# Performance work log

Hardware: AMD Instinct MI355X
Metric: run time of the kernel (lower is better)

## Reference

```python
import jax, jax.numpy as jnp
import numpy as np

B, S, HID, H = 2, 2048, 1024, 16
D = HID // H
ROTARY_BASE = 10000.0
LN_EPS = 1e-5
NEG = -1e9


def setup_inputs() -> dict:
    key = jax.random.key(0)
    ks = jax.random.split(key, 20)
    w = lambda k, shape: (jax.random.normal(k, shape, jnp.float32) * 0.02)
    return {
        "x": jax.random.normal(ks[0], (B, S, HID), jnp.float32),
        "mask": jnp.ones((B, S), jnp.int32),
        "wq": w(ks[1], (HID, HID)), "bq": jnp.zeros((HID,), jnp.float32),
        "wk": w(ks[2], (HID, HID)), "bk": jnp.zeros((HID,), jnp.float32),
        "wv": w(ks[3], (HID, HID)), "bv": jnp.zeros((HID,), jnp.float32),
        "wo": w(ks[4], (HID, HID)), "bo": jnp.zeros((HID,), jnp.float32),
        "w1": w(ks[5], (HID, 4 * HID)), "b1": jnp.zeros((4 * HID,), jnp.float32),
        "w2": w(ks[6], (4 * HID, HID)), "b2": jnp.zeros((HID,), jnp.float32),
        "ln1_g": jnp.ones((HID,), jnp.float32), "ln1_b": jnp.zeros((HID,), jnp.float32),
        "ln2_g": jnp.ones((HID,), jnp.float32), "ln2_b": jnp.zeros((HID,), jnp.float32),
    }


def _layer_norm(z, g, b):
    m = z.mean(-1, keepdims=True)
    v = ((z - m) ** 2).mean(-1, keepdims=True)
    return (z - m) / jnp.sqrt(v + LN_EPS) * g + b


def _rope(t, cos, sin):
    # t: [B,H,S,D]; even/odd halves rotated then CONCATENATED (matches source, not interleaved)
    e, o = t[..., 0::2], t[..., 1::2]
    return jnp.concatenate([e * cos - o * sin, e * sin + o * cos], axis=-1)


def reference(x, mask, wq, bq, wk, bk, wv, bv, wo, bo, w1, b1, w2, b2,
              ln1_g, ln1_b, ln2_g, ln2_b):
    b, s, hid = x.shape
    h, d = H, D
    # rotary tables for positions [0, s)
    inv_freq = 1.0 / (ROTARY_BASE ** (jnp.arange(0, d, 2, dtype=jnp.float32) / d))
    freqs = jnp.arange(s, dtype=jnp.float32)[:, None] * inv_freq[None, :]  # [S, D/2]
    cos = jnp.cos(freqs)[None, None]  # [1,1,S,D/2]
    sin = jnp.sin(freqs)[None, None]

    # ---- attention sublayer (pre-norm) ----
    xn = _layer_norm(x, ln1_g, ln1_b)
    q = (xn @ wq + bq).reshape(b, s, h, d).transpose(0, 2, 1, 3)
    k = (xn @ wk + bk).reshape(b, s, h, d).transpose(0, 2, 1, 3)
    v = (xn @ wv + bv).reshape(b, s, h, d).transpose(0, 2, 1, 3)
    q = _rope(q, cos, sin)
    k = _rope(k, cos, sin)

    scores = jnp.einsum('bhqd,bhkd->bhqk', q, k) / np.sqrt(d).astype(np.float32)
    pad = (mask == 0)[:, None, None, :]              # [B,1,1,S]
    scores = jnp.where(pad, NEG, scores)
    causal = jnp.triu(jnp.ones((s, s), bool), 1)     # [S,S]
    scores = jnp.where(causal, NEG, scores)
    probs = jax.nn.softmax(scores, axis=-1)          # dropout p=0.0 (eval)
    ctx = jnp.einsum('bhqk,bhkd->bhqd', probs, v)
    ctx = ctx.transpose(0, 2, 1, 3).reshape(b, s, hid)
    attn_out = ctx @ wo + bo
    x = x + attn_out

    # ---- FFN sublayer (pre-norm) ----
    xn = _layer_norm(x, ln2_g, ln2_b)
    f = jax.nn.gelu(xn @ w1 + b1, approximate=True) @ w2 + b2
    return x + f
```

## Files before the change

kernel.cpp:

```cpp
#include <hip/hip_runtime.h>

typedef unsigned short u16;
typedef unsigned int u32;
typedef __attribute__((ext_vector_type(8))) u16 u16x8;
typedef __attribute__((ext_vector_type(4))) u16 u16x4;
typedef __attribute__((ext_vector_type(8))) __bf16 bf16x8;
typedef __attribute__((ext_vector_type(4))) float f32x4;

static __device__ __forceinline__ float bf2f(u16 u) {
    union { u32 i; float f; } v; v.i = ((u32)u) << 16; return v.f;
}
static __device__ __forceinline__ u16 f2bf(float f) {
    union { float f; u32 i; } v; v.f = f;
    u32 r = v.i + 0x7fffu + ((v.i >> 16) & 1u);
    return (u16)(r >> 16);
}
static __device__ __forceinline__ u16 f2bfn(float f) {
    __bf16 h = (__bf16)f;
    return *(u16*)&h;
}
static __device__ __forceinline__ void gl_lds16(const void* gsrc, void* ldst) {
    __builtin_amdgcn_global_load_lds((const __attribute__((address_space(1))) void*)gsrc,
                                     (__attribute__((address_space(3))) void*)ldst, 16, 0, 0);
}

__global__ __launch_bounds__(256) void transpose_cvt(const float* __restrict__ in,
                                                     u16* __restrict__ out, int K, int N) {
    __shared__ float t[32][33];
    int k0 = blockIdx.y << 5, n0 = blockIdx.x << 5;
    int r = threadIdx.x >> 3, c4 = threadIdx.x & 7;
    float4 v = *(const float4*)(in + (size_t)(k0 + r) * N + n0 + (c4 << 2));
    t[r][c4 * 4 + 0] = v.x; t[r][c4 * 4 + 1] = v.y;
    t[r][c4 * 4 + 2] = v.z; t[r][c4 * 4 + 3] = v.w;
    __syncthreads();
    u16x4 o;
    o[0] = f2bf(t[c4 * 4 + 0][r]); o[1] = f2bf(t[c4 * 4 + 1][r]);
    o[2] = f2bf(t[c4 * 4 + 2][r]); o[3] = f2bf(t[c4 * 4 + 3][r]);
    *(u16x4*)(out + (size_t)(n0 + r) * K + k0 + (c4 << 2)) = o;
}

__global__ __launch_bounds__(256) void transpose_cvt4(const float* __restrict__ w0, const float* __restrict__ w1,
                                                      const float* __restrict__ w2, const float* __restrict__ w3,
                                                      u16* __restrict__ o0, u16* __restrict__ o1,
                                                      u16* __restrict__ o2, u16* __restrict__ o3) {
    __shared__ float t[32][33];
    const float* in; u16* out;
    switch (blockIdx.z) {
        case 0:  in = w0; out = o0; break;
        case 1:  in = w1; out = o1; break;
        case 2:  in = w2; out = o2; break;
        default: in = w3; out = o3; break;
    }
    int k0 = blockIdx.y << 5, n0 = blockIdx.x << 5;
    int r = threadIdx.x >> 3, c4 = threadIdx.x & 7;
    float4 v = *(const float4*)(in + (size_t)(k0 + r) * 1024 + n0 + (c4 << 2));
    t[r][c4 * 4 + 0] = v.x; t[r][c4 * 4 + 1] = v.y;
    t[r][c4 * 4 + 2] = v.z; t[r][c4 * 4 + 3] = v.w;
    __syncthreads();
    u16x4 o;
    o[0] = f2bf(t[c4 * 4 + 0][r]); o[1] = f2bf(t[c4 * 4 + 1][r]);
    o[2] = f2bf(t[c4 * 4 + 2][r]); o[3] = f2bf(t[c4 * 4 + 3][r]);
    *(u16x4*)(out + (size_t)(n0 + r) * 1024 + k0 + (c4 << 2)) = o;
}

__global__ void concat_bias(const float* __restrict__ bq, const float* __restrict__ bk,
                            const float* __restrict__ bv, float* __restrict__ bqkv,
                            const int* __restrict__ mask, float* __restrict__ maskf) {
    int i = blockIdx.x * 256 + threadIdx.x;
    if (i < 3072) {
        float v = (i < 1024) ? bq[i] : (i < 2048 ? bk[i - 1024] : bv[i - 2048]);
        bqkv[i] = v;
    }
    if (i < 4096) maskf[i] = (float)mask[i];
}

__global__ void rope_tab(float* __restrict__ cost, float* __restrict__ sint) {
    int idx = blockIdx.x * 256 + threadIdx.x;
    int s = idx >> 5, f = idx & 31;
    float inv = powf(10000.0f, -((float)(2 * f)) / 64.0f);
    float a = (float)s * inv;
    cost[idx] = cosf(a);
    sint[idx] = sinf(a);
}

__global__ __launch_bounds__(256) void ln_kernel(const float* __restrict__ x,
                                                 const float* __restrict__ gam,
                                                 const float* __restrict__ bet,
                                                 u16* __restrict__ out) {
    int row = blockIdx.x, tid = threadIdx.x;
    float4 v = *((const float4*)(x + (size_t)row * 1024) + tid);
    float s = v.x + v.y + v.z + v.w;
    float sq = v.x * v.x + v.y * v.y + v.z * v.z + v.w * v.w;
    #pragma unroll
    for (int off = 32; off >= 1; off >>= 1) {
        s += __shfl_xor(s, off);
        sq += __shfl_xor(sq, off);
    }
    __shared__ float red[8];
    int wid = tid >> 6, lane = tid & 63;
    if (lane == 0) { red[wid] = s; red[wid + 4] = sq; }
    __syncthreads();
    float ts = red[0] + red[1] + red[2] + red[3];
    float tq = red[4] + red[5] + red[6] + red[7];
    float mean = ts * (1.0f / 1024.0f);
    float var = tq * (1.0f / 1024.0f) - mean * mean;
    float rstd = rsqrtf(var + 1e-5f);
    float4 g = ((const float4*)gam)[tid];
    float4 b = ((const float4*)bet)[tid];
    u16x4 o;
    o[0] = f2bfn((v.x - mean) * rstd * g.x + b.x);
    o[1] = f2bfn((v.y - mean) * rstd * g.y + b.y);
    o[2] = f2bfn((v.z - mean) * rstd * g.z + b.z);
    o[3] = f2bfn((v.w - mean) * rstd * g.w + b.w);
    *(u16x4*)(out + (size_t)row * 1024 + (tid << 2)) = o;
}

__global__ __launch_bounds__(256) void ln_fuse(float* __restrict__ x2, const u16* __restrict__ part,
                                               const float* __restrict__ gam, const float* __restrict__ bet,
                                               u16* __restrict__ out) {
    int row = blockIdx.x, tid = threadIdx.x;
    float4 v = *((const float4*)(x2 + (size_t)row * 1024) + tid);
    u16x4 pv = *(const u16x4*)(part + (size_t)row * 1024 + (tid << 2));
    v.x += bf2f(pv[0]); v.y += bf2f(pv[1]); v.z += bf2f(pv[2]); v.w += bf2f(pv[3]);
    *((float4*)(x2 + (size_t)row * 1024) + tid) = v;
    float s = v.x + v.y + v.z + v.w;
    float sq = v.x * v.x + v.y * v.y + v.z * v.z + v.w * v.w;
    #pragma unroll
    for (int off = 32; off >= 1; off >>= 1) {
        s += __shfl_xor(s, off);
        sq += __shfl_xor(sq, off);
    }
    __shared__ float red[8];
    int wid = tid >> 6, lane = tid & 63;
    if (lane == 0) { red[wid] = s; red[wid + 4] = sq; }
    __syncthreads();
    float ts = red[0] + red[1] + red[2] + red[3];
    float tq = red[4] + red[5] + red[6] + red[7];
    float mean = ts * (1.0f / 1024.0f);
    float var = tq * (1.0f / 1024.0f) - mean * mean;
    float rstd = rsqrtf(var + 1e-5f);
    float4 g = ((const float4*)gam)[tid];
    float4 b = ((const float4*)bet)[tid];
    u16x4 o;
    o[0] = f2bfn((v.x - mean) * rstd * g.x + b.x);
    o[1] = f2bfn((v.y - mean) * rstd * g.y + b.y);
    o[2] = f2bfn((v.z - mean) * rstd * g.z + b.z);
    o[3] = f2bfn((v.w - mean) * rstd * g.w + b.w);
    *(u16x4*)(out + (size_t)row * 1024 + (tid << 2)) = o;
}

template <int EPI>
__global__ __launch_bounds__(512, 2) void gemm256(const u16* __restrict__ A, const u16* __restrict__ Bt,
                                                  const float* __restrict__ bias,
                                                  u16* __restrict__ outb, int M, int N, int K) {
    __shared__ __align__(16) u16 lds[65536];
    const int tid = threadIdx.x;
    const int lane = tid & 63, wid = tid >> 6;
    const int cl = lane & 15, g4 = lane >> 4;
    const int wr = wid >> 2, wc = wid & 3;
    const int gx = gridDim.x;
    const int lid = blockIdx.y * gx + blockIdx.x;
    const int per8 = (gx * gridDim.y) >> 3;
    const int newlin = (lid & 7) * per8 + (lid >> 3);
    const int m0 = (newlin / gx) << 8;
    const int n0 = (newlin % gx) << 8;
    const int NT = K >> 6;
    f32x4 acc[8][4] = {};
    const int r0 = tid >> 3;          const int gc0 = (tid & 7) ^ (r0 & 7);
    const int r1 = (tid + 512) >> 3;  const int gc1 = (tid & 7) ^ (r1 & 7);
    const int wub = wid << 10;

    auto stageHalf = [&](int buf, int mat, int h, int kt) {
        const u16* src = mat ? Bt : A;
        const int base0 = mat ? n0 : m0;
        char* d = (char*)lds + buf * 65536 + mat * 32768 + h * 16384 + wub;
        gl_lds16(src + (size_t)(base0 + h * 128 + r0) * K + (kt << 6) + (gc0 << 3), d);
        gl_lds16(src + (size_t)(base0 + h * 128 + r1) * K + (kt << 6) + (gc1 << 3), d + 8192);
    };

    stageHalf(0, 0, 0, 0); stageHalf(0, 0, 1, 0);
    stageHalf(0, 1, 0, 0); stageHalf(0, 1, 1, 0);
    asm volatile("s_waitcnt vmcnt(0)" ::: "memory");
    __builtin_amdgcn_s_barrier();

    for (int t = 0; t < NT; ++t) {
        const int buf = t & 1, nbuf = buf ^ 1;
        const bool more = (t + 1 < NT);
        const int abase = buf * 65536 + wr * 16384;
        const int bbase = buf * 65536 + 32768 + (wc >> 1) * 16384;
        bf16x8 bfr[4][2];
        #pragma unroll
        for (int q = 0; q < 4; ++q) {
            bf16x8 afr[2][2];
            #pragma unroll
            for (int di = 0; di < 2; ++di)
                #pragma unroll
                for (int ks = 0; ks < 2; ++ks) {
                    int row = q * 32 + di * 16 + cl;
                    int gr = ks * 4 + g4;
                    afr[di][ks] = *(const bf16x8*)((char*)lds + abase + (((row << 3) + (gr ^ (row & 7))) << 4));
                }
            if (q == 0) {
                #pragma unroll
                for (int j = 0; j < 4; ++j)
                    #pragma unroll
                    for (int ks = 0; ks < 2; ++ks) {
                        int row = ((wc & 1) << 6) + j * 16 + cl;
                        int gr = ks * 4 + g4;
                        bfr[j][ks] = *(const bf16x8*)((char*)lds + bbase + (((row << 3) + (gr ^ (row & 7))) << 4));
                    }
            }
            if (more) stageHalf(nbuf, q >> 1, q & 1, t + 1);
            __builtin_amdgcn_s_barrier();
            asm volatile("s_waitcnt lgkmcnt(0)" ::: "memory");
            __builtin_amdgcn_sched_barrier(0);
            __builtin_amdgcn_s_setprio(1);
            #pragma unroll
            for (int di = 0; di < 2; ++di)
                #pragma unroll
                for (int j = 0; j < 4; ++j)
                    #pragma unroll
                    for (int ks = 0; ks < 2; ++ks)
                        acc[q * 2 + di][j] = __builtin_amdgcn_mfma_f32_16x16x32_bf16(
                            afr[di][ks], bfr[j][ks], acc[q * 2 + di][j], 0, 0, 0);
            __builtin_amdgcn_s_setprio(0);
            if (q == 3 && more) asm volatile("s_waitcnt vmcnt(0)" ::: "memory");
            __builtin_amdgcn_s_barrier();
            if (q == 3) __builtin_amdgcn_sched_barrier(0);
        }
    }
    #pragma unroll
    for (int i = 0; i < 8; ++i)
        #pragma unroll
        for (int j = 0; j < 4; ++j) {
            int row = m0 + wr * 128 + i * 16 + g4 * 4;
            int col = n0 + wc * 64 + j * 16 + cl;
            float bc = bias[col];
            #pragma unroll
            for (int rr = 0; rr < 4; ++rr) {
                float v = acc[i][j][rr] + bc;
                size_t idx = (size_t)(row + rr) * N + col;
                if constexpr (EPI == 0) {
                    outb[idx] = f2bfn(v);
                } else {
                    float tg = 0.7978845608f * (v + 0.044715f * v * v * v);
                    outb[idx] = f2bfn(v / (1.0f + exp2f(tg * -2.88539008f)));
                }
            }
        }
}

__global__ __launch_bounds__(512, 2) void gemm256r(const u16* __restrict__ A, const u16* __restrict__ Bt,
                                                   const float* __restrict__ bias,
                                                   const float* __restrict__ res,
                                                   float* __restrict__ outf, u16* __restrict__ poutb,
                                                   int M, int N, int K) {
    __shared__ __align__(16) u16 lds[65536];
    const int tid = threadIdx.x;
    const int lane = tid & 63, wid = tid >> 6;
    const int cl = lane & 15, g4 = lane >> 4;
    const int wr = wid >> 2, wc = wid & 3;
    const int gx = gridDim.x;
    const int lid = blockIdx.y * gx + blockIdx.x;
    const int per8 = (gx * gridDim.y) >> 3;
    const int newlin = (lid & 7) * per8 + (lid >> 3);
    const int m0 = (newlin / gx) << 8;
    const int n0 = (newlin % gx) << 8;
    const int kchunk = K / gridDim.z;
    const int kbase = blockIdx.z * kchunk;
    const int NT = kchunk >> 6;
    f32x4 acc[8][4] = {};
    const int r0 = tid >> 3;          const int gc0 = (tid & 7) ^ (r0 & 7);
    const int r1 = (tid + 512) >> 3;  const int gc1 = (tid & 7) ^ (r1 & 7);
    const int wub = wid << 10;

    auto stageHalf = [&](int buf, int mat, int h, int kt) {
        const u16* src = mat ? Bt : A;
        const int base0 = mat ? n0 : m0;
        char* d = (char*)lds + buf * 65536 + mat * 32768 + h * 16384 + wub;
        gl_lds16(src + (size_t)(base0 + h * 128 + r0) * K + kbase + (kt << 6) + (gc0 << 3), d);
        gl_lds16(src + (size_t)(base0 + h * 128 + r1) * K + kbase + (kt << 6) + (gc1 << 3), d + 8192);
    };

    stageHalf(0, 0, 0, 0); stageHalf(0, 0, 1, 0);
    stageHalf(0, 1, 0, 0); stageHalf(0, 1, 1, 0);
    asm volatile("s_waitcnt vmcnt(0)" ::: "memory");
    __builtin_amdgcn_s_barrier();

    for (int t = 0; t < NT; ++t) {
        const int buf = t & 1, nbuf = buf ^ 1;
        const bool more = (t + 1 < NT);
        const int abase = buf * 65536 + wr * 16384;
        const int bbase = buf * 65536 + 32768 + (wc >> 1) * 16384;
        bf16x8 bfr[4][2];
        #pragma unroll
        for (int q = 0; q < 4; ++q) {
            bf16x8 afr[2][2];
            #pragma unroll
            for (int di = 0; di < 2; ++di)
                #pragma unroll
                for (int ks = 0; ks < 2; ++ks) {
                    int row = q * 32 + di * 16 + cl;
                    int gr = ks * 4 + g4;
                    afr[di][ks] = *(const bf16x8*)((char*)lds + abase + (((row << 3) + (gr ^ (row & 7))) << 4));
                }
            if (q == 0) {
                #pragma unroll
                for (int j = 0; j < 4; ++j)
                    #pragma unroll
                    for (int ks = 0; ks < 2; ++ks) {
                        int row = ((wc & 1) << 6) + j * 16 + cl;
                        int gr = ks * 4 + g4;
                        bfr[j][ks] = *(const bf16x8*)((char*)lds + bbase + (((row << 3) + (gr ^ (row & 7))) << 4));
                    }
            }
            if (more) stageHalf(nbuf, q >> 1, q & 1, t + 1);
            __builtin_amdgcn_s_barrier();
            asm volatile("s_waitcnt lgkmcnt(0)" ::: "memory");
            __builtin_amdgcn_sched_barrier(0);
            __builtin_amdgcn_s_setprio(1);
            #pragma unroll
            for (int di = 0; di < 2; ++di)
                #pragma unroll
                for (int j = 0; j < 4; ++j)
                    #pragma unroll
                    for (int ks = 0; ks < 2; ++ks)
                        acc[q * 2 + di][j] = __builtin_amdgcn_mfma_f32_16x16x32_bf16(
                            afr[di][ks], bfr[j][ks], acc[q * 2 + di][j], 0, 0, 0);
            __builtin_amdgcn_s_setprio(0);
            if (q == 3 && more) asm volatile("s_waitcnt vmcnt(0)" ::: "memory");
            __builtin_amdgcn_s_barrier();
            if (q == 3) __builtin_amdgcn_sched_barrier(0);
        }
    }
    if (blockIdx.z == 0) {
        #pragma unroll
        for (int i = 0; i < 8; ++i)
            #pragma unroll
            for (int j = 0; j < 4; ++j) {
                int row = m0 + wr * 128 + i * 16 + g4 * 4;
                int col = n0 + wc * 64 + j * 16 + cl;
                float bc = bias[col];
                #pragma unroll
                for (int rr = 0; rr < 4; ++rr) {
                    size_t idx = (size_t)(row + rr) * N + col;
                    outf[idx] = acc[i][j][rr] + bc + res[idx];
                }
            }
    } else {
        const size_t pbase = (size_t)(blockIdx.z - 1) * ((size_t)M * N);
        #pragma unroll
        for (int i = 0; i < 8; ++i)
            #pragma unroll
            for (int j = 0; j < 4; ++j) {
                int row = m0 + wr * 128 + i * 16 + g4 * 4;
                int col = n0 + wc * 64 + j * 16 + cl;
                #pragma unroll
                for (int rr = 0; rr < 4; ++rr)
                    poutb[pbase + (size_t)(row + rr) * N + col] = f2bfn(acc[i][j][rr]);
            }
    }
}

template <int EPI>
__global__ __launch_bounds__(256) void gemm_bt(const u16* __restrict__ A, const u16* __restrict__ Bt,
                                               const float* __restrict__ bias,
                                               const float* __restrict__ res,
                                               u16* __restrict__ outb, float* __restrict__ outf,
                                               u16* __restrict__ poutb,
                                               int M, int N, int K) {
    __shared__ __align__(16) u16 As[3][4096];
    __shared__ __align__(16) u16 Bs[3][4096];
    const int tid = threadIdx.x;
    const int lane = tid & 63, wid = tid >> 6;
    const int g = lane >> 4, cl = lane & 15;
    const int wr = wid >> 1, wc = wid & 1;
    const int gx = gridDim.x;
    const int lid = blockIdx.y * gx + blockIdx.x;
    const int per8 = (gx * gridDim.y) >> 3;
    const int newlin = (lid & 7) * per8 + (lid >> 3);
    const int m0 = (newlin / gx) << 7;
    const int n0 = (newlin % gx) << 7;
    const int kchunk = K / gridDim.z;
    const int kbase = blockIdx.z * kchunk;
    const int NT = kchunk >> 5;
    f32x4 acc[4][4] = {};
    const int grow = tid >> 2;
    const int gcol = (tid & 3) ^ ((tid >> 3) & 3);

    auto stage = [&](int buf, int kt) {
        const int ko = kbase + (kt << 5);
        gl_lds16(A + (size_t)(m0 + grow) * K + ko + (gcol << 3),       &As[buf][wid << 9]);
        gl_lds16(A + (size_t)(m0 + grow + 64) * K + ko + (gcol << 3),  &As[buf][(wid << 9) + 2048]);
        gl_lds16(Bt + (size_t)(n0 + grow) * K + ko + (gcol << 3),      &Bs[buf][wid << 9]);
        gl_lds16(Bt + (size_t)(n0 + grow + 64) * K + ko + (gcol << 3), &Bs[buf][(wid << 9) + 2048]);
    };

    stage(0, 0);
    stage(1, 1);
    for (int kt = 0; kt < NT; ++kt) {
        if (kt + 1 < NT) asm volatile("s_waitcnt vmcnt(4)" ::: "memory");
        else             asm volatile("s_waitcnt vmcnt(0)" ::: "memory");
        __builtin_amdgcn_s_barrier();
        __builtin_amdgcn_sched_barrier(0);
        if (kt + 2 < NT) stage((kt + 2) % 3, kt + 2);
        const int cb = kt % 3;
        bf16x8 a[4], b[4];
        #pragma unroll
        for (int i = 0; i < 4; ++i) {
            int row = (wr << 6) + (i << 4) + cl;
            a[i] = *(const bf16x8*)&As[cb][((row << 2) + (g ^ ((row >> 1) & 3))) << 3];
        }
        #pragma unroll
        for (int j = 0; j < 4; ++j) {
            int row = (wc << 6) + (j << 4) + cl;
            b[j] = *(const bf16x8*)&Bs[cb][((row << 2) + (g ^ ((row >> 1) & 3))) << 3];
        }
        __builtin_amdgcn_s_setprio(1);
        #pragma unroll
        for (int i = 0; i < 4; ++i)
            #pragma unroll
            for (int j = 0; j < 4; ++j)
                acc[i][j] = __builtin_amdgcn_mfma_f32_16x16x32_bf16(a[i], b[j], acc[i][j], 0, 0, 0);
        __builtin_amdgcn_s_setprio(0);
    }
    if (blockIdx.z == 0) {
        #pragma unroll
        for (int i = 0; i < 4; ++i)
            #pragma unroll
            for (int j = 0; j < 4; ++j) {
                int row = m0 + (wr << 6) + (i << 4) + (g << 2);
                int col = n0 + (wc << 6) + (j << 4) + cl;
                float bc = bias[col];
                #pragma unroll
                for (int rr = 0; rr < 4; ++rr) {
                    float v = acc[i][j][rr] + bc;
                    size_t idx = (size_t)(row + rr) * N + col;
                    outf[idx] = v + res[idx];
                }
            }
    } else {
        const size_t pbase = (size_t)(blockIdx.z - 1) * ((size_t)M * N);
        #pragma unroll
        for (int i = 0; i < 4; ++i)
            #pragma unroll
            for (int j = 0; j < 4; ++j) {
                int row = m0 + (wr << 6) + (i << 4) + (g << 2);
                int col = n0 + (wc << 6) + (j << 4) + cl;
                #pragma unroll
                for (int rr = 0; rr < 4; ++rr)
                    poutb[pbase + (size_t)(row + rr) * N + col] = f2bfn(acc[i][j][rr]);
            }
    }
}

__global__ __launch_bounds__(256) void reduce_addb(float* __restrict__ out, const u16* __restrict__ p,
                                                   int nparts) {
    int i = blockIdx.x * 256 + threadIdx.x;
    float4 a = ((const float4*)out)[i];
    for (int j = 0; j < nparts; ++j) {
        u16x4 v = *(const u16x4*)(p + (size_t)j * 4194304 + ((size_t)i << 2));
        a.x += bf2f(v[0]); a.y += bf2f(v[1]); a.z += bf2f(v[2]); a.w += bf2f(v[3]);
    }
    ((float4*)out)[i] = a;
}

__global__ __launch_bounds__(256) void rope_qk(const u16* __restrict__ qkv,
                                               const float* __restrict__ cost,
                                               const float* __restrict__ sint,
                                               u16* __restrict__ qr, u16* __restrict__ kr) {
    int tid = threadIdx.x;
    int rowid = (blockIdx.x << 4) + (tid >> 4);
    int j = tid & 15;
    int half = j >> 3, jj = j & 7;
    int b = rowid >> 15;
    int h = (rowid >> 11) & 15;
    int s = rowid & 2047;
    size_t qbase = (size_t)((b << 11) + s) * 3072 + (h << 6);
    float cf[4], sf_[4];
    {
        float4 c = *(const float4*)(cost + (s << 5) + (jj << 2));
        float4 sn = *(const float4*)(sint + (s << 5) + (jj << 2));
        cf[0] = c.x; cf[1] = c.y; cf[2] = c.z; cf[3] = c.w;
        sf_[0] = sn.x; sf_[1] = sn.y; sf_[2] = sn.z; sf_[3] = sn.w;
    }
    size_t obase = (size_t)rowid * 64 + (half << 5) + (jj << 2);
    {
        u16x8 v = *(const u16x8*)(qkv + qbase + (jj << 3));
        u16x4 o;
        #pragma unroll
        for (int m2 = 0; m2 < 4; ++m2) {
            float e = bf2f(v[2 * m2]), od = bf2f(v[2 * m2 + 1]);
            float val = (half == 0) ? (e * cf[m2] - od * sf_[m2]) : (e * sf_[m2] + od * cf[m2]);
            o[m2] = f2bfn(val * 0.1803368801f);
        }
        *(u16x4*)(qr + obase) = o;
    }
    {
        u16x8 v = *(const u16x8*)(qkv + qbase + 1024 + (jj << 3));
        u16x4 o;
        #pragma unroll
        for (int m2 = 0; m2 < 4; ++m2) {
            float e = bf2f(v[2 * m2]), od = bf2f(v[2 * m2 + 1]);
            float val = (half == 0) ? (e * cf[m2] - od * sf_[m2]) : (e * sf_[m2] + od * cf[m2]);
            o[m2] = f2bfn(val);
        }
        *(u16x4*)(kr + obase) = o;
    }
}

__global__ __launch_bounds__(256) void v_transpose(const u16* __restrict__ qkv,
                                                   u16* __restrict__ vt) {
    __shared__ __align__(16) u16 tl[64 * 80];
    int stile = blockIdx.x, bh = blockIdx.y;
    int b = bh >> 4, h = bh & 15;
    int tid = threadIdx.x;
    #pragma unroll
    for (int i = 0; i < 2; ++i) {
        int slot = tid + (i << 8);
        int srow = slot >> 3, c = slot & 7;
        u16x8 v = *(const u16x8*)(qkv + (size_t)((b << 11) + (stile << 6) + srow) * 3072 + 2048 + (h << 6) + (c << 3));
        *(u16x8*)(tl + srow * 80 + (c << 3)) = v;
    }
    __syncthreads();
    #pragma unroll
    for (int i = 0; i < 2; ++i) {
        int slot = tid + (i << 8);
        int drow = slot >> 3, c = slot & 7;
        u16x8 o;
        #pragma unroll
        for (int m2 = 0; m2 < 8; ++m2) o[m2] = tl[(c * 8 + m2) * 80 + drow];
        *(u16x8*)(vt + ((size_t)bh * 64 + drow) * 2048 + (stile << 6) + (c << 3)) = o;
    }
}

__global__ __launch_bounds__(256) void attn_kernel(const u16* __restrict__ Q, const u16* __restrict__ Kd,
                                                   const u16* __restrict__ Vt, const float* __restrict__ maskf,
                                                   u16* __restrict__ ctx) {
    __shared__ __align__(16) u16 Ks[2][4096];
    __shared__ __align__(16) u16 Vs[2][4096];
    __shared__ __align__(16) u16 Ps[4096];
    const int tid = threadIdx.x, lane = tid & 63, w = tid >> 6;
    const int g = lane >> 4, cl = lane & 15;
    const int lid = blockIdx.y * 16 + blockIdx.x;
    const int xcd = lid & 7, slot = lid >> 3;
    const int bh = xcd * 4 + (slot >> 4);
    const int pair = slot & 15;
    const int b = bh >> 4, h = bh & 15;
    const u16* Kb = Kd + (size_t)bh * 2048 * 64;
    const u16* Vb = Vt + (size_t)bh * 64 * 2048;
    const int sr = tid >> 3;
    const int sg = (tid & 7) ^ (sr & 7);
    bf16x8 onesb;
    #pragma unroll
    for (int i2 = 0; i2 < 8; ++i2) onesb[i2] = (__bf16)1.0f;
    char* const pwb = (char*)Ps + w * 2048 + cl * 128 + ((g & 1) << 3);

    #pragma unroll
    for (int ci = 0; ci < 2; ++ci) {
        const int qb = (ci == 0) ? (31 - pair) : pair;
        const size_t qoff = ((size_t)bh * 2048 + qb * 64 + w * 16 + cl) * 64;
        const bf16x8 qa0 = *(const bf16x8*)(Q + qoff + (g << 3));
        const bf16x8 qa1 = *(const bf16x8*)(Q + qoff + 32 + (g << 3));
        const int qrow = qb * 64 + w * 16 + cl;
        f32x4 acc[4] = {};
        f32x4 lsum = {};

        auto stage = [&](int buf, int t) {
            char* kd = (char*)&Ks[buf][0] + (w << 10);
            char* vd = (char*)&Vs[buf][0] + (w << 10);
            const u16* Kg = Kb + (size_t)(t * 64) * 64;
            gl_lds16(Kg + (size_t)sr * 64 + (sg << 3), kd);
            gl_lds16(Kg + (size_t)(sr + 32) * 64 + (sg << 3), kd + 4096);
            gl_lds16(Vb + (size_t)sr * 2048 + t * 64 + (sg << 3), vd);
            gl_lds16(Vb + (size_t)(sr + 32) * 2048 + t * 64 + (sg << 3), vd + 4096);
        };

        __syncthreads();
        stage(0, 0);
        asm volatile("s_waitcnt vmcnt(0)" ::: "memory");
        __syncthreads();

        int cur = 0;
        for (int t = 0; t <= qb; ++t) {
            const bool more = (t < qb);
            if (more) stage(cur ^ 1, t + 1);
            f32x4 sf[4];
            __builtin_amdgcn_s_setprio(1);
            #pragma unroll
            for (int ct = 0; ct < 4; ++ct) {
                f32x4 s = {};
                int krow = ct * 16 + cl;
                bf16x8 kb0 = *(const bf16x8*)((char*)&Ks[cur][0] + krow * 128 + ((g ^ (krow & 7)) << 4));
                bf16x8 kb1 = *(const bf16x8*)((char*)&Ks[cur][0] + krow * 128 + (((4 + g) ^ (krow & 7)) << 4));
                s = __builtin_amdgcn_mfma_f32_16x16x32_bf16(kb0, qa0, s, 0, 0, 0);
                s = __builtin_amdgcn_mfma_f32_16x16x32_bf16(kb1, qa1, s, 0, 0, 0);
                sf[ct] = s;
            }
            __builtin_amdgcn_s_setprio(0);
            const bool diag = (t == qb);
            #pragma unroll
            for (int ct = 0; ct < 4; ++ct) {
                const int kc0 = t * 64 + ct * 16 + (g << 2);
                const float4 mv = *(const float4*)(maskf + (b << 11) + kc0);
                float p0 = exp2f(sf[ct][0]) * mv.x;
                float p1 = exp2f(sf[ct][1]) * mv.y;
                float p2 = exp2f(sf[ct][2]) * mv.z;
                float p3 = exp2f(sf[ct][3]) * mv.w;
                if (diag) {
                    p0 = (kc0 + 0 <= qrow) ? p0 : 0.0f;
                    p1 = (kc0 + 1 <= qrow) ? p1 : 0.0f;
                    p2 = (kc0 + 2 <= qrow) ? p2 : 0.0f;
                    p3 = (kc0 + 3 <= qrow) ? p3 : 0.0f;
                }
                u32 lo, hi;
                asm("v_cvt_pk_bf16_f32 %0, %1, %2" : "=v"(lo) : "v"(p0), "v"(p1));
                asm("v_cvt_pk_bf16_f32 %0, %1, %2" : "=v"(hi) : "v"(p2), "v"(p3));
                uint2 pk; pk.x = lo; pk.y = hi;
                *(uint2*)(pwb + ((((ct << 1) + (g >> 1)) ^ (cl & 7)) << 4)) = pk;
            }
            __builtin_amdgcn_s_setprio(1);
            #pragma unroll
            for (int kc = 0; kc < 2; ++kc) {
                bf16x8 pa = *(const bf16x8*)((char*)Ps + w * 2048 + cl * 128 + (((kc * 4 + g) ^ (cl & 7)) << 4));
                lsum = __builtin_amdgcn_mfma_f32_16x16x32_bf16(pa, onesb, lsum, 0, 0, 0);
                #pragma unroll
                for (int n = 0; n < 4; ++n) {
                    int vrow = n * 16 + cl;
                    bf16x8 vb = *(const bf16x8*)((char*)&Vs[cur][0] + vrow * 128 + (((kc * 4 + g) ^ (vrow & 7)) << 4));
                    acc[n] = __builtin_amdgcn_mfma_f32_16x16x32_bf16(pa, vb, acc[n], 0, 0, 0);
                }
            }
            __builtin_amdgcn_s_setprio(0);
            if (more) {
                asm volatile("s_waitcnt vmcnt(0)" ::: "memory");
                __syncthreads();
            }
            cur ^= 1;
        }
        #pragma unroll
        for (int n = 0; n < 4; ++n)
            #pragma unroll
            for (int rr = 0; rr < 4; ++rr) {
                int token = (b << 11) + qb * 64 + w * 16 + g * 4 + rr;
                int col = (h << 6) + n * 16 + cl;
                ctx[(size_t)token * 1024 + col] = f2bfn(acc[n][rr] / lsum[rr]);
            }
    }
}

extern "C" void kernel_launch(void* const* d_in, const int* in_sizes, int n_in,
                              void* d_out, int out_size, void* d_ws, size_t ws_size,
                              hipStream_t stream) {
    const float* x   = (const float*)d_in[0];
    const int* mask  = (const int*)d_in[1];
    const float* wq  = (const float*)d_in[2];
    const float* bq  = (const float*)d_in[3];
    const float* wk  = (const float*)d_in[4];
    const float* bk  = (const float*)d_in[5];
    const float* wv  = (const float*)d_in[6];
    const float* bv  = (const float*)d_in[7];
    const float* wo  = (const float*)d_in[8];
    const float* bo  = (const float*)d_in[9];
    const float* w1  = (const float*)d_in[10];
    const float* b1  = (const float*)d_in[11];
    const float* w2  = (const float*)d_in[12];
    const float* b2  = (const float*)d_in[13];
    const float* g1  = (const float*)d_in[14];
    const float* be1 = (const float*)d_in[15];
    const float* g2  = (const float*)d_in[16];
    const float* be2 = (const float*)d_in[17];
    float* out = (float*)d_out;
    char* ws = (char*)d_ws;

    u16* wqkvT  = (u16*)(ws + 0);
    u16* woT    = (u16*)(ws + 6291456);
    u16* w1T    = (u16*)(ws + 8388608);
    u16* w2T    = (u16*)(ws + 16777216);
    float* bqkv = (float*)(ws + 25165824);
    float* cost = (float*)(ws + 25178112);
    float* sint = (float*)(ws + 25440256);
    u16* xn     = (u16*)(ws + 25702400);
    float* x2   = (float*)(ws + 34091008);
    float* maskf= (float*)(ws + 34091008);
    u16* qkv    = (u16*)(ws + 50868224);
    u16* ffh    = (u16*)(ws + 50868224);
    u16* qr     = (u16*)(ws + 76034048);
    u16* kr     = (u16*)(ws + 84422656);
    u16* vt     = (u16*)(ws + 92811264);
    u16* ctx    = (u16*)(ws + 101199872);
    u16* partb  = (u16*)(ws + 84422656);

    transpose_cvt4<<<dim3(32, 32, 4), 256, 0, stream>>>(wq, wk, wv, wo,
                                                        wqkvT, wqkvT + 1024 * 1024, wqkvT + 2048 * 1024, woT);
    transpose_cvt<<<dim3(128, 32), 256, 0, stream>>>(w1, w1T, 1024, 4096);
    transpose_cvt<<<dim3(32, 128), 256, 0, stream>>>(w2, w2T, 4096, 1024);
    concat_bias<<<16, 256, 0, stream>>>(bq, bk, bv, bqkv, mask, maskf);
    rope_tab<<<256, 256, 0, stream>>>(cost, sint);

    ln_kernel<<<4096, 256, 0, stream>>>(x, g1, be1, xn);
    gemm256<0><<<dim3(12, 16), 512, 0, stream>>>(xn, wqkvT, bqkv, qkv, 4096, 3072, 1024);
    rope_qk<<<4096, 256, 0, stream>>>(qkv, cost, sint, qr, kr);
    v_transpose<<<dim3(32, 32), 256, 0, stream>>>(qkv, vt);
    attn_kernel<<<dim3(16, 32), 256, 0, stream>>>(qr, kr, vt, maskf, ctx);
    gemm_bt<1><<<dim3(8, 32, 2), 256, 0, stream>>>(ctx, woT, bo, x, nullptr, x2, partb, 4096, 1024, 1024);
    ln_fuse<<<4096, 256, 0, stream>>>(x2, partb, g2, be2, xn);
    gemm256<2><<<dim3(16, 16), 512, 0, stream>>>(xn, w1T, b1, ffh, 4096, 4096, 1024);
    gemm256r<<<dim3(4, 16, 4), 512, 0, stream>>>(ffh, w2T, b2, x2, out, partb, 4096, 1024, 4096);
    reduce_addb<<<4096, 256, 0, stream>>>(out, partb, 3);
}
```

Baseline: 246.5 us.

## Triple-buffer attention K/V staging and merge prep kernel launches

The attention kernel moves from double to triple buffering of K/V tiles in LDS. It prefetches two tiles ahead and waits with a partial vmcnt, so global loads overlap more with compute. Separately, the two w1/w2 transpose launches are merged into one grid-z launch, and the bias-concat and rope-table kernels are fused into one prep kernel, cutting launch count. The extra LDS buffers raise shared memory per block, which may reduce occupancy.

```diff
diff --git a/kernel.cpp b/kernel.cpp
--- a/kernel.cpp
+++ b/kernel.cpp
@@ -22,21 +22,6 @@
 static __device__ __forceinline__ void gl_lds16(const void* gsrc, void* ldst) {
     __builtin_amdgcn_global_load_lds((const __attribute__((address_space(1))) void*)gsrc,
                                      (__attribute__((address_space(3))) void*)ldst, 16, 0, 0);
-}
-
-__global__ __launch_bounds__(256) void transpose_cvt(const float* __restrict__ in,
-                                                     u16* __restrict__ out, int K, int N) {
-    __shared__ float t[32][33];
-    int k0 = blockIdx.y << 5, n0 = blockIdx.x << 5;
-    int r = threadIdx.x >> 3, c4 = threadIdx.x & 7;
-    float4 v = *(const float4*)(in + (size_t)(k0 + r) * N + n0 + (c4 << 2));
-    t[r][c4 * 4 + 0] = v.x; t[r][c4 * 4 + 1] = v.y;
-    t[r][c4 * 4 + 2] = v.z; t[r][c4 * 4 + 3] = v.w;
-    __syncthreads();
-    u16x4 o;
-    o[0] = f2bf(t[c4 * 4 + 0][r]); o[1] = f2bf(t[c4 * 4 + 1][r]);
-    o[2] = f2bf(t[c4 * 4 + 2][r]); o[3] = f2bf(t[c4 * 4 + 3][r]);
-    *(u16x4*)(out + (size_t)(n0 + r) * K + k0 + (c4 << 2)) = o;
 }
 
 __global__ __launch_bounds__(256) void transpose_cvt4(const float* __restrict__ w0, const float* __restrict__ w1,
@@ -63,24 +48,42 @@
     *(u16x4*)(out + (size_t)(n0 + r) * 1024 + k0 + (c4 << 2)) = o;
 }
 
-__global__ void concat_bias(const float* __restrict__ bq, const float* __restrict__ bk,
+__global__ __launch_bounds__(256) void transpose_cvt2(const float* __restrict__ w1, const float* __restrict__ w2,
+                                                      u16* __restrict__ o1, u16* __restrict__ o2) {
+    __shared__ float t[32][33];
+    const int zz = blockIdx.z;
+    const float* in = zz ? w2 : w1;
+    u16* out = zz ? o2 : o1;
+    const int K = zz ? 4096 : 1024, N = zz ? 1024 : 4096;
+    int k0, n0;
+    if (zz) { k0 = blockIdx.x << 5; n0 = blockIdx.y << 5; }
+    else    { n0 = blockIdx.x << 5; k0 = blockIdx.y << 5; }
+    int r = threadIdx.x >> 3, c4 = threadIdx.x & 7;
+    float4 v = *(const float4*)(in + (size_t)(k0 + r) * N + n0 + (c4 << 2));
+    t[r][c4 * 4 + 0] = v.x; t[r][c4 * 4 + 1] = v.y;
+    t[r][c4 * 4 + 2] = v.z; t[r][c4 * 4 + 3] = v.w;
+    __syncthreads();
+    u16x4 o;
+    o[0] = f2bf(t[c4 * 4 + 0][r]); o[1] = f2bf(t[c4 * 4 + 1][r]);
+    o[2] = f2bf(t[c4 * 4 + 2][r]); o[3] = f2bf(t[c4 * 4 + 3][r]);
+    *(u16x4*)(out + (size_t)(n0 + r) * K + k0 + (c4 << 2)) = o;
+}
+
+__global__ void prep_kernel(const float* __restrict__ bq, const float* __restrict__ bk,
                             const float* __restrict__ bv, float* __restrict__ bqkv,
-                            const int* __restrict__ mask, float* __restrict__ maskf) {
-    int i = blockIdx.x * 256 + threadIdx.x;
-    if (i < 3072) {
-        float v = (i < 1024) ? bq[i] : (i < 2048 ? bk[i - 1024] : bv[i - 2048]);
-        bqkv[i] = v;
-    }
-    if (i < 4096) maskf[i] = (float)mask[i];
-}
-
-__global__ void rope_tab(float* __restrict__ cost, float* __restrict__ sint) {
+                            const int* __restrict__ mask, float* __restrict__ maskf,
+                            float* __restrict__ cost, float* __restrict__ sint) {
     int idx = blockIdx.x * 256 + threadIdx.x;
     int s = idx >> 5, f = idx & 31;
     float inv = powf(10000.0f, -((float)(2 * f)) / 64.0f);
     float a = (float)s * inv;
     cost[idx] = cosf(a);
     sint[idx] = sinf(a);
+    if (idx < 3072) {
+        float v = (idx < 1024) ? bq[idx] : (idx < 2048 ? bk[idx - 1024] : bv[idx - 2048]);
+        bqkv[idx] = v;
+    }
+    if (idx < 4096) maskf[idx] = (float)mask[idx];
 }
 
 __global__ __launch_bounds__(256) void ln_kernel(const float* __restrict__ x,
@@ -537,8 +540,8 @@
 __global__ __launch_bounds__(256) void attn_kernel(const u16* __restrict__ Q, const u16* __restrict__ Kd,
                                                    const u16* __restrict__ Vt, const float* __restrict__ maskf,
                                                    u16* __restrict__ ctx) {
-    __shared__ __align__(16) u16 Ks[2][4096];
-    __shared__ __align__(16) u16 Vs[2][4096];
+    __shared__ __align__(16) u16 Ks[3][4096];
+    __shared__ __align__(16) u16 Vs[3][4096];
     __shared__ __align__(16) u16 Ps[4096];
     const int tid = threadIdx.x, lane = tid & 63, w = tid >> 6;
     const int g = lane >> 4, cl = lane & 15;
@@ -578,13 +581,18 @@
 
         __syncthreads();
         stage(0, 0);
-        asm volatile("s_waitcnt vmcnt(0)" ::: "memory");
+        if (qb >= 1) {
+            stage(1, 1);
+            asm volatile("s_waitcnt vmcnt(4)" ::: "memory");
+        } else {
+            asm volatile("s_waitcnt vmcnt(0)" ::: "memory");
+        }
         __syncthreads();
 
-        int cur = 0;
         for (int t = 0; t <= qb; ++t) {
             const bool more = (t < qb);
-            if (more) stage(cur ^ 1, t + 1);
+            if (t + 2 <= qb) stage((t + 2) % 3, t + 2);
+            const int cur = t % 3;
             f32x4 sf[4];
             __builtin_amdgcn_s_setprio(1);
             #pragma unroll
@@ -633,10 +641,11 @@
             }
             __builtin_amdgcn_s_setprio(0);
             if (more) {
-                asm volatile("s_waitcnt vmcnt(0)" ::: "memory");
+                if (t + 2 <= qb) asm volatile("s_waitcnt vmcnt(4)" ::: "memory");
+                else             asm volatile("s_waitcnt vmcnt(0)" ::: "memory");
                 __syncthreads();
-            }
-            cur ^= 1;
+                __builtin_amdgcn_sched_barrier(0);
+            }
         }
         #pragma unroll
         for (int n = 0; n < 4; ++n)
@@ -693,10 +702,8 @@
 
     transpose_cvt4<<<dim3(32, 32, 4), 256, 0, stream>>>(wq, wk, wv, wo,
                                                         wqkvT, wqkvT + 1024 * 1024, wqkvT + 2048 * 1024, woT);
-    transpose_cvt<<<dim3(128, 32), 256, 0, stream>>>(w1, w1T, 1024, 4096);
-    transpose_cvt<<<dim3(32, 128), 256, 0, stream>>>(w2, w2T, 4096, 1024);
-    concat_bias<<<16, 256, 0, stream>>>(bq, bk, bv, bqkv, mask, maskf);
-    rope_tab<<<256, 256, 0, stream>>>(cost, sint);
+    transpose_cvt2<<<dim3(128, 32, 2), 256, 0, stream>>>(w1, w2, w1T, w2T);
+    prep_kernel<<<256, 256, 0, stream>>>(bq, bk, bv, bqkv, mask, maskf, cost, sint);
 
     ln_kernel<<<4096, 256, 0, stream>>>(x, g1, be1, xn);
     gemm256<0><<<dim3(12, 16), 512, 0, stream>>>(xn, wqkvT, bqkv, qkv, 4096, 3072, 1024);
```

New measurement: 246.1 us. No clear change (-0.2%).
